# Kernel optimization log

Measured on AMD Instinct MI355X. Metric: run time of the kernel, lower is better.

## Reference

```python
import jax, jax.numpy as jnp
import numpy as np

B, N, E = 4, 1024, 16
S = 4  # num species
AH = PH = 64  # hidden dims


def _mlp(x, W0, b0, W1, b1, W2, b2):
    h = jax.nn.silu(x @ W0 + b0)
    h = jax.nn.silu(h @ W1 + b1)
    return h @ W2 + b2  # [..., 1]


def setup_inputs() -> dict:
    key = jax.random.key(0)
    ks = jax.random.split(key, 20)
    scale = 0.1
    inp = {
        "positions": jax.random.normal(ks[0], (B, N, 2), jnp.float32),
        "species": jax.random.randint(ks[1], (B, N), 0, S, jnp.int32),
        "electric_field": jax.random.normal(ks[2], (B, 2), jnp.float32),
        "embed": jax.random.normal(ks[3], (S, E), jnp.float32) * scale,
        "aW0": jax.random.normal(ks[4], (2 + 2 + 1 + E, AH), jnp.float32) * scale,
        "ab0": jax.random.normal(ks[5], (AH,), jnp.float32) * scale,
        "aW1": jax.random.normal(ks[6], (AH, AH), jnp.float32) * scale,
        "ab1": jax.random.normal(ks[7], (AH,), jnp.float32) * scale,
        "aW2": jax.random.normal(ks[8], (AH, 1), jnp.float32) * scale,
        "ab2": jax.random.normal(ks[9], (1,), jnp.float32) * scale,
        "pW0": jax.random.normal(ks[10], (2 + 1 + 1 + 1 + 2 * E, PH), jnp.float32) * scale,
        "pb0": jax.random.normal(ks[11], (PH,), jnp.float32) * scale,
        "pW1": jax.random.normal(ks[12], (PH, PH), jnp.float32) * scale,
        "pb1": jax.random.normal(ks[13], (PH,), jnp.float32) * scale,
        "pW2": jax.random.normal(ks[14], (PH, 1), jnp.float32) * scale,
        "pb2": jax.random.normal(ks[15], (1,), jnp.float32) * scale,
    }
    return inp


def reference(positions, species, electric_field, embed,
              aW0, ab0, aW1, ab1, aW2, ab2,
              pW0, pb0, pW1, pb1, pW2, pb2):
    num_atoms = positions.shape[1]
    cp = positions - positions.mean(axis=1, keepdims=True)         # [B,N,2]
    semb = embed[species]                                          # [B,N,E]
    e_norm = jnp.linalg.norm(electric_field, axis=-1, keepdims=True)  # [B,1]

    # atom channel
    atom_field = jnp.broadcast_to(electric_field[:, None, :], (cp.shape[0], num_atoms, 2))
    atom_enorm = jnp.broadcast_to(e_norm[:, None, :], (cp.shape[0], num_atoms, 1))
    atom_feat = jnp.concatenate([cp, atom_field, atom_enorm, semb], axis=-1)
    atom_energy = _mlp(atom_feat, aW0, ab0, aW1, ab1, aW2, ab2)[..., 0].sum(axis=1)

    # pair channel: all i<j pairs, fully vectorized
    i_idx, j_idx = jnp.triu_indices(num_atoms, k=1)                # [P]
    rij = cp[:, i_idx, :] - cp[:, j_idx, :]                        # [B,P,2]
    dij = jnp.linalg.norm(rij, axis=-1, keepdims=True)             # [B,P,1]
    uij = rij / jnp.maximum(dij, 1e-12)
    e_dot_u = jnp.sum(electric_field[:, None, :] * uij, axis=-1, keepdims=True)
    pair_enorm = jnp.broadcast_to(e_norm[:, None, :], dij.shape)
    pair_feat = jnp.concatenate(
        [rij, dij, e_dot_u, pair_enorm, semb[:, i_idx, :], semb[:, j_idx, :]], axis=-1)
    pair_energy = _mlp(pair_feat, pW0, pb0, pW1, pb1, pW2, pb2)[..., 0].sum(axis=1)

    return atom_energy + pair_energy
```

## Files before the change

kernel.cpp:

```cpp
#include <hip/hip_runtime.h>

#define NA 1024
#define NBATCH 4
#define NPAIR 523776
#define PAIR_TILES 2046
#define PAIR_BLOCKS 511
#define GRID_X 512

#define LOG2E_F 1.44269504088896f
#define LN2_F   0.69314718055995f

#define WS_MEAN 0
#define WS_W0P  64
#define WS_W0A  2112
#define WS_W1P  4160
#define WS_W1A  12352

typedef _Float16 half4 __attribute__((ext_vector_type(4)));
typedef _Float16 half8 __attribute__((ext_vector_type(8)));
typedef __fp16 fp16x2 __attribute__((ext_vector_type(2)));
typedef float float4v __attribute__((ext_vector_type(4)));

#if defined(__has_builtin)
#  if __has_builtin(__builtin_amdgcn_exp2f)
#    define EXP2F(x) __builtin_amdgcn_exp2f(x)
#  endif
#endif
#ifndef EXP2F
#  define EXP2F(x) exp2f(x)
#endif

__device__ __forceinline__ float4v sig4(float4v y) {
    float4v e;
#pragma unroll
    for (int r = 0; r < 4; r++) e[r] = EXP2F(-y[r]);
    float4v d = e + 1.0f;
    float4v rr;
#pragma unroll
    for (int r = 0; r < 4; r++) rr[r] = __builtin_amdgcn_rcpf(d[r]);
    return rr;
}

__device__ __forceinline__ uint32_t pkf16(float a, float b) {
    union { _Float16 h[2]; uint32_t u; } x;
    x.h[0] = (_Float16)a; x.h[1] = (_Float16)b;
    return x.u;
}

__global__ void prep_kernel(const float* __restrict__ positions,
                            const float* __restrict__ embed,
                            const float* __restrict__ aW0,
                            const float* __restrict__ ab0,
                            const float* __restrict__ aW1,
                            const float* __restrict__ ab2,
                            const float* __restrict__ pW0,
                            const float* __restrict__ pb0,
                            const float* __restrict__ pW1,
                            const float* __restrict__ pb2,
                            char* __restrict__ ws,
                            float* __restrict__ out) {
    const int tid = threadIdx.x;
    if (blockIdx.x < 4) {
        const int b = blockIdx.x;
        const float2* pos = (const float2*)positions + b * NA;
        float sx = 0.f, sy = 0.f;
        for (int t = tid; t < NA; t += 256) {
            float2 p = pos[t];
            sx += p.x; sy += p.y;
        }
#pragma unroll
        for (int off = 32; off > 0; off >>= 1) {
            sx += __shfl_down(sx, off);
            sy += __shfl_down(sy, off);
        }
        __shared__ float rxs[4], rys[4];
        const int w = tid >> 6, lane = tid & 63;
        if (lane == 0) { rxs[w] = sx; rys[w] = sy; }
        __syncthreads();
        if (tid == 0) {
            float* meanws = (float*)(ws + WS_MEAN);
            meanws[b * 2 + 0] = (rxs[0] + rxs[1] + rxs[2] + rxs[3]) * (1.f / NA);
            meanws[b * 2 + 1] = (rys[0] + rys[1] + rys[2] + rys[3]) * (1.f / NA);
            out[b] = (float)NPAIR * pb2[0] + (float)NA * ab2[0];
        }
        return;
    }

    _Float16* w0p = (_Float16*)(ws + WS_W0P);
    _Float16* w0a = (_Float16*)(ws + WS_W0A);
    _Float16* w1p = (_Float16*)(ws + WS_W1P);
    _Float16* w1a = (_Float16*)(ws + WS_W1A);

    for (int idx = tid; idx < 1024; idx += 256) {
        const int j = idx & 3, lane = (idx >> 2) & 63, nt = idx >> 8;
        const int k = ((lane >> 4) << 2) + j;
        const int col = nt * 16 + (lane & 15);
        float vp = 0.f, va = 0.f;
        if (k < 5) {
            vp = pW0[k * 64 + col];
            va = aW0[k * 64 + col];
        } else if (k == 5) {
            vp = pb0[col];
            va = ab0[col];
        } else if (k >= 6 && k <= 9) {
            const int s = k - 6;
            float accp = 0.f, acca = 0.f;
#pragma unroll
            for (int e = 0; e < 16; e++) {
                float em = embed[s * 16 + e];
                accp += em * pW0[(5 + e) * 64 + col];
                acca += em * aW0[(5 + e) * 64 + col];
            }
            vp = accp; va = acca;
        } else if (k >= 10 && k <= 13) {
            const int s = k - 10;
            float accp = 0.f;
#pragma unroll
            for (int e = 0; e < 16; e++)
                accp += embed[s * 16 + e] * pW0[(21 + e) * 64 + col];
            vp = accp; va = 0.f;
        }
        w0p[idx] = (_Float16)(vp * LOG2E_F);
        w0a[idx] = (_Float16)(va * LOG2E_F);
    }
    for (int idx = tid; idx < 4096; idx += 256) {
        const int j = idx & 7, lane = (idx >> 3) & 63;
        const int ks = (idx >> 9) & 1, nt = idx >> 10;
        const int q = lane >> 4;
        const int m = (j < 4) ? (4 * q + j) : (16 + 4 * q + (j - 4));
        const int k = ks * 32 + m;
        const int col = nt * 16 + (lane & 15);
        w1p[idx] = (_Float16)pW1[k * 64 + col];
        w1a[idx] = (_Float16)aW1[k * 64 + col];
    }
}

__global__ __launch_bounds__(256, 4) void mlp_kernel(
    const float* __restrict__ positions,
    const int*   __restrict__ species,
    const float* __restrict__ efield,
    const float* __restrict__ ab1, const float* __restrict__ aW2,
    const float* __restrict__ pb1, const float* __restrict__ pW2,
    const char*  __restrict__ ws,
    float* __restrict__ out)
{
    const int b    = blockIdx.y;
    const int bx   = blockIdx.x;
    const bool is_atom = (bx == PAIR_BLOCKS);
    const int tid  = threadIdx.x;
    const int lane = tid & 63;
    const int wv   = tid >> 6;
    const int n16  = lane & 15;
    const int quad = lane >> 4;

    __shared__ __attribute__((aligned(16))) _Float16 Xbuf[4][64][24];
    _Float16 (*rows)[24] = Xbuf[wv];

    const _Float16* w0w = (const _Float16*)(ws + (is_atom ? WS_W0A : WS_W0P));
    const _Float16* w1w = (const _Float16*)(ws + (is_atom ? WS_W1A : WS_W1P));
    half4 w0f[4];
    half8 w1f[4][2];
#pragma unroll
    for (int nt = 0; nt < 4; nt++)
        w0f[nt] = *(const half4*)(w0w + (nt * 64 + lane) * 4);
#pragma unroll
    for (int nt = 0; nt < 4; nt++)
#pragma unroll
        for (int ks = 0; ks < 2; ks++)
            w1f[nt][ks] = *(const half8*)(w1w + ((nt * 2 + ks) * 64 + lane) * 8);

    const float* B1 = is_atom ? ab1 : pb1;
    float4v b1q[4];
#pragma unroll
    for (int nt = 0; nt < 4; nt++) {
        float4v t4 = *(const float4v*)(B1 + nt * 16 + quad * 4);
        b1q[nt] = t4 * LOG2E_F;
    }

    const float Ex = efield[b * 2 + 0];
    const float Ey = efield[b * 2 + 1];
    const float enorm = sqrtf(Ex * Ex + Ey * Ey);
    const float* meanws = (const float*)(ws + WS_MEAN);
    const float mnx = meanws[b * 2 + 0];
    const float mny = meanws[b * 2 + 1];

    const uint32_t enorm_pack = pkf16(enorm, 1.0f);
    const uint32_t ef_pack    = pkf16(Ex, Ey);

    const int my_tiles = is_atom ? 4 : ((bx < PAIR_TILES - 4 * PAIR_BLOCKS) ? 5 : 4);

    const float4v zero4 = {0.f, 0.f, 0.f, 0.f};
    float4v acce[4];
#pragma unroll
    for (int nt = 0; nt < 4; nt++) acce[nt] = zero4;

    for (int t = 0; t < my_tiles; ++t) {
        uint32_t w01, w23;
        uint64_t ohi, ohj;
        if (!is_atom) {
            const int tile = bx + t * PAIR_BLOCKS;
            const int p = tile * 256 + tid;
            const float s = sqrtf((float)(2047 * 2047 - 8 * p));
            int i = (int)((2047.0f - s) * 0.5f);
            i = i < 0 ? 0 : (i > 1022 ? 1022 : i);
            const int j = p - ((i * (2047 - i)) >> 1) + i + 1;
            const float2* pos = (const float2*)positions + b * NA;
            float2 pi = pos[i], pj = pos[j];
            float f0 = pi.x - pj.x, f1 = pi.y - pj.y;
            float f2 = sqrtf(f0 * f0 + f1 * f1);
            float inv = __builtin_amdgcn_rcpf(fmaxf(f2, 1e-12f));
            float f3 = (Ex * f0 + Ey * f1) * inv;
            w01 = pkf16(f0, f1);
            w23 = pkf16(f2, f3);
            ohi = 0x3C00ull << (species[b * NA + i] * 16);
            ohj = 0x3C00ull << (species[b * NA + j] * 16);
        } else {
            const int n = t * 256 + tid;
            float2 pn = ((const float2*)positions)[b * NA + n];
            w01 = pkf16(pn.x - mnx, pn.y - mny);
            w23 = ef_pack;
            ohi = 0x3C00ull << (species[b * NA + n] * 16);
            ohj = 0;
        }
        int4* dst = (int4*)&rows[lane][0];
        int4 lo, hi;
        lo.x = (int)w01;
        lo.y = (int)w23;
        lo.z = (int)enorm_pack;
        lo.w = (int)(uint32_t)ohi;
        hi.x = (int)(uint32_t)(ohi >> 32);
        hi.y = (int)(uint32_t)ohj;
        hi.z = (int)(uint32_t)(ohj >> 32);
        hi.w = 0;
        dst[0] = lo;
        dst[1] = hi;

        half4 xfr[4];
#pragma unroll
        for (int mt = 0; mt < 4; mt++)
            xfr[mt] = *(const half4*)(&rows[mt * 16 + n16][quad * 4]);

#pragma unroll
        for (int mt = 0; mt < 4; mt++) {
            float4v acc[4];
#pragma unroll
            for (int nt = 0; nt < 4; nt++)
                acc[nt] = __builtin_amdgcn_mfma_f32_16x16x16f16(
                    w0f[nt], xfr[mt], zero4, 0, 0, 0);

            float4v s0 = acc[0] * sig4(acc[0]);
            float4v s1 = acc[1] * sig4(acc[1]);
            float4v s2 = acc[2] * sig4(acc[2]);
            float4v s3 = acc[3] * sig4(acc[3]);
            union { half8 h8; fp16x2 h2[4]; } u0, u1;
            u0.h2[0] = __builtin_amdgcn_cvt_pkrtz(s0[0], s0[1]);
            u0.h2[1] = __builtin_amdgcn_cvt_pkrtz(s0[2], s0[3]);
            u0.h2[2] = __builtin_amdgcn_cvt_pkrtz(s1[0], s1[1]);
            u0.h2[3] = __builtin_amdgcn_cvt_pkrtz(s1[2], s1[3]);
            u1.h2[0] = __builtin_amdgcn_cvt_pkrtz(s2[0], s2[1]);
            u1.h2[1] = __builtin_amdgcn_cvt_pkrtz(s2[2], s2[3]);
            u1.h2[2] = __builtin_amdgcn_cvt_pkrtz(s3[0], s3[1]);
            u1.h2[3] = __builtin_amdgcn_cvt_pkrtz(s3[2], s3[3]);

#pragma unroll
            for (int nt = 0; nt < 4; nt++) {
                float4v c = b1q[nt];
                c = __builtin_amdgcn_mfma_f32_16x16x32_f16(w1f[nt][0], u0.h8, c, 0, 0, 0);
                c = __builtin_amdgcn_mfma_f32_16x16x32_f16(w1f[nt][1], u1.h8, c, 0, 0, 0);
                acce[nt] += c * sig4(c);
            }
        }
    }

    const float* W2 = is_atom ? aW2 : pW2;
    float4v dot4 = {0.f, 0.f, 0.f, 0.f};
#pragma unroll
    for (int nt = 0; nt < 4; nt++) {
        float4v w2v4 = *(const float4v*)(W2 + nt * 16 + quad * 4);
        dot4 += acce[nt] * w2v4;
    }
    float energy = (dot4[0] + dot4[1] + dot4[2] + dot4[3]) * LN2_F;

#pragma unroll
    for (int off = 32; off > 0; off >>= 1)
        energy += __shfl_down(energy, off);
    __shared__ float wsum[4];
    if (lane == 0) wsum[wv] = energy;
    __syncthreads();
    if (tid == 0)
        atomicAdd(&out[b], wsum[0] + wsum[1] + wsum[2] + wsum[3]);
}

extern "C" void kernel_launch(void* const* d_in, const int* in_sizes, int n_in,
                              void* d_out, int out_size, void* d_ws, size_t ws_size,
                              hipStream_t stream) {
    const float* positions = (const float*)d_in[0];
    const int*   species   = (const int*)  d_in[1];
    const float* efield    = (const float*)d_in[2];
    const float* embed     = (const float*)d_in[3];
    const float* aW0 = (const float*)d_in[4];
    const float* ab0 = (const float*)d_in[5];
    const float* aW1 = (const float*)d_in[6];
    const float* ab1 = (const float*)d_in[7];
    const float* aW2 = (const float*)d_in[8];
    const float* ab2 = (const float*)d_in[9];
    const float* pW0 = (const float*)d_in[10];
    const float* pb0 = (const float*)d_in[11];
    const float* pW1 = (const float*)d_in[12];
    const float* pb1 = (const float*)d_in[13];
    const float* pW2 = (const float*)d_in[14];
    const float* pb2 = (const float*)d_in[15];
    float* outp = (float*)d_out;
    char*  ws   = (char*)d_ws;

    prep_kernel<<<dim3(5), dim3(256), 0, stream>>>(
        positions, embed, aW0, ab0, aW1, ab2, pW0, pb0, pW1, pb2, ws, outp);
    mlp_kernel<<<dim3(GRID_X, NBATCH), dim3(256), 0, stream>>>(
        positions, species, efield,
        ab1, aW2, pb1, pW2,
        ws, outp);
}
```

Baseline: 152.7 us.

## Software-pipeline pair tile loads and LDS staging across MLP compute

Restructures the tile loop so the global loads of positions and species for the next tile are issued before the current tile's MFMA work. The LDS row write and fragment reads for that next tile are interleaved between the per-row-block MLP bodies, overlapping memory latency with matrix and sigmoid math. It also replaces the packed round-toward-zero f16 conversions with plain casts. In exchange it keeps more registers live per thread, which could lower occupancy, and the new casts may emit more conversion instructions.

```diff
diff --git a/kernel.cpp b/kernel.cpp
--- a/kernel.cpp
+++ b/kernel.cpp
@@ -18,7 +18,6 @@
 
 typedef _Float16 half4 __attribute__((ext_vector_type(4)));
 typedef _Float16 half8 __attribute__((ext_vector_type(8)));
-typedef __fp16 fp16x2 __attribute__((ext_vector_type(2)));
 typedef float float4v __attribute__((ext_vector_type(4)));
 
 #if defined(__has_builtin)
@@ -184,6 +183,9 @@
     const float mnx = meanws[b * 2 + 0];
     const float mny = meanws[b * 2 + 1];
 
+    const float2* pos = (const float2*)positions + b * NA;
+    const int*    spc = species + b * NA;
+
     const uint32_t enorm_pack = pkf16(enorm, 1.0f);
     const uint32_t ef_pack    = pkf16(Ex, Ey);
 
@@ -194,83 +196,106 @@
 #pragma unroll
     for (int nt = 0; nt < 4; nt++) acce[nt] = zero4;
 
+    half4 xfr[4];
+
+#define LOADRAW(TT, o_pi, o_pj, o_si, o_sj) do {                              \
+        if (!is_atom) {                                                       \
+            const int p_ = (bx + (TT) * PAIR_BLOCKS) * 256 + tid;             \
+            const float sq_ = sqrtf((float)(2047 * 2047 - 8 * p_));           \
+            int i_ = (int)((2047.0f - sq_) * 0.5f);                           \
+            i_ = i_ < 0 ? 0 : (i_ > 1022 ? 1022 : i_);                        \
+            const int j_ = p_ - ((i_ * (2047 - i_)) >> 1) + i_ + 1;           \
+            o_pi = pos[i_]; o_pj = pos[j_];                                   \
+            o_si = spc[i_]; o_sj = spc[j_];                                   \
+        } else {                                                              \
+            const int n_ = (TT) * 256 + tid;                                  \
+            o_pi = pos[n_]; o_si = spc[n_];                                   \
+        }                                                                     \
+    } while (0)
+
+#define PACKWRITE(i_pi, i_pj, i_si, i_sj) do {                                \
+        uint32_t w01_, w23_; uint64_t ohi_, ohj_;                             \
+        if (!is_atom) {                                                       \
+            float f0_ = i_pi.x - i_pj.x, f1_ = i_pi.y - i_pj.y;               \
+            float f2_ = sqrtf(f0_ * f0_ + f1_ * f1_);                         \
+            float inv_ = __builtin_amdgcn_rcpf(fmaxf(f2_, 1e-12f));           \
+            float f3_ = (Ex * f0_ + Ey * f1_) * inv_;                         \
+            w01_ = pkf16(f0_, f1_); w23_ = pkf16(f2_, f3_);                   \
+            ohi_ = 0x3C00ull << (i_si * 16);                                  \
+            ohj_ = 0x3C00ull << (i_sj * 16);                                  \
+        } else {                                                              \
+            w01_ = pkf16(i_pi.x - mnx, i_pi.y - mny);                         \
+            w23_ = ef_pack;                                                   \
+            ohi_ = 0x3C00ull << (i_si * 16);                                  \
+            ohj_ = 0;                                                         \
+        }                                                                     \
+        int4* dst_ = (int4*)&rows[lane][0];                                   \
+        int4 lo_, hi_;                                                        \
+        lo_.x = (int)w01_; lo_.y = (int)w23_;                                 \
+        lo_.z = (int)enorm_pack; lo_.w = (int)(uint32_t)ohi_;                 \
+        hi_.x = (int)(uint32_t)(ohi_ >> 32); hi_.y = (int)(uint32_t)ohj_;     \
+        hi_.z = (int)(uint32_t)(ohj_ >> 32); hi_.w = 0;                       \
+        dst_[0] = lo_; dst_[1] = hi_;                                         \
+    } while (0)
+
+#define READXFR_ONE(MT)                                                       \
+    xfr[MT] = *(const half4*)(&rows[(MT) * 16 + n16][quad * 4])
+
+#define MTBODY(MT) do {                                                       \
+        float4v acc_[4];                                                      \
+        _Pragma("unroll")                                                     \
+        for (int nt = 0; nt < 4; nt++)                                        \
+            acc_[nt] = __builtin_amdgcn_mfma_f32_16x16x16f16(                 \
+                w0f[nt], xfr[MT], zero4, 0, 0, 0);                            \
+        float4v s0_ = acc_[0] * sig4(acc_[0]);                                \
+        float4v s1_ = acc_[1] * sig4(acc_[1]);                                \
+        float4v s2_ = acc_[2] * sig4(acc_[2]);                                \
+        float4v s3_ = acc_[3] * sig4(acc_[3]);                                \
+        half8 h0_, h1_;                                                       \
+        _Pragma("unroll")                                                     \
+        for (int r = 0; r < 4; r++) {                                         \
+            h0_[r]     = (_Float16)s0_[r];                                    \
+            h0_[4 + r] = (_Float16)s1_[r];                                    \
+            h1_[r]     = (_Float16)s2_[r];                                    \
+            h1_[4 + r] = (_Float16)s3_[r];                                    \
+        }                                                                     \
+        _Pragma("unroll")                                                     \
+        for (int nt = 0; nt < 4; nt++) {                                      \
+            float4v c_ = b1q[nt];                                             \
+            c_ = __builtin_amdgcn_mfma_f32_16x16x32_f16(w1f[nt][0], h0_, c_, 0, 0, 0); \
+            c_ = __builtin_amdgcn_mfma_f32_16x16x32_f16(w1f[nt][1], h1_, c_, 0, 0, 0); \
+            acce[nt] += c_ * sig4(c_);                                        \
+        }                                                                     \
+    } while (0)
+
+    {
+        float2 c_pi, c_pj; int c_si = 0, c_sj = 0;
+        LOADRAW(0, c_pi, c_pj, c_si, c_sj);
+        PACKWRITE(c_pi, c_pj, c_si, c_sj);
+        READXFR_ONE(0); READXFR_ONE(1); READXFR_ONE(2); READXFR_ONE(3);
+    }
+
     for (int t = 0; t < my_tiles; ++t) {
-        uint32_t w01, w23;
-        uint64_t ohi, ohj;
-        if (!is_atom) {
-            const int tile = bx + t * PAIR_BLOCKS;
-            const int p = tile * 256 + tid;
-            const float s = sqrtf((float)(2047 * 2047 - 8 * p));
-            int i = (int)((2047.0f - s) * 0.5f);
-            i = i < 0 ? 0 : (i > 1022 ? 1022 : i);
-            const int j = p - ((i * (2047 - i)) >> 1) + i + 1;
-            const float2* pos = (const float2*)positions + b * NA;
-            float2 pi = pos[i], pj = pos[j];
-            float f0 = pi.x - pj.x, f1 = pi.y - pj.y;
-            float f2 = sqrtf(f0 * f0 + f1 * f1);
-            float inv = __builtin_amdgcn_rcpf(fmaxf(f2, 1e-12f));
-            float f3 = (Ex * f0 + Ey * f1) * inv;
-            w01 = pkf16(f0, f1);
-            w23 = pkf16(f2, f3);
-            ohi = 0x3C00ull << (species[b * NA + i] * 16);
-            ohj = 0x3C00ull << (species[b * NA + j] * 16);
-        } else {
-            const int n = t * 256 + tid;
-            float2 pn = ((const float2*)positions)[b * NA + n];
-            w01 = pkf16(pn.x - mnx, pn.y - mny);
-            w23 = ef_pack;
-            ohi = 0x3C00ull << (species[b * NA + n] * 16);
-            ohj = 0;
-        }
-        int4* dst = (int4*)&rows[lane][0];
-        int4 lo, hi;
-        lo.x = (int)w01;
-        lo.y = (int)w23;
-        lo.z = (int)enorm_pack;
-        lo.w = (int)(uint32_t)ohi;
-        hi.x = (int)(uint32_t)(ohi >> 32);
-        hi.y = (int)(uint32_t)ohj;
-        hi.z = (int)(uint32_t)(ohj >> 32);
-        hi.w = 0;
-        dst[0] = lo;
-        dst[1] = hi;
-
-        half4 xfr[4];
-#pragma unroll
-        for (int mt = 0; mt < 4; mt++)
-            xfr[mt] = *(const half4*)(&rows[mt * 16 + n16][quad * 4]);
-
-#pragma unroll
-        for (int mt = 0; mt < 4; mt++) {
-            float4v acc[4];
-#pragma unroll
-            for (int nt = 0; nt < 4; nt++)
-                acc[nt] = __builtin_amdgcn_mfma_f32_16x16x16f16(
-                    w0f[nt], xfr[mt], zero4, 0, 0, 0);
-
-            float4v s0 = acc[0] * sig4(acc[0]);
-            float4v s1 = acc[1] * sig4(acc[1]);
-            float4v s2 = acc[2] * sig4(acc[2]);
-            float4v s3 = acc[3] * sig4(acc[3]);
-            union { half8 h8; fp16x2 h2[4]; } u0, u1;
-            u0.h2[0] = __builtin_amdgcn_cvt_pkrtz(s0[0], s0[1]);
-            u0.h2[1] = __builtin_amdgcn_cvt_pkrtz(s0[2], s0[3]);
-            u0.h2[2] = __builtin_amdgcn_cvt_pkrtz(s1[0], s1[1]);
-            u0.h2[3] = __builtin_amdgcn_cvt_pkrtz(s1[2], s1[3]);
-            u1.h2[0] = __builtin_amdgcn_cvt_pkrtz(s2[0], s2[1]);
-            u1.h2[1] = __builtin_amdgcn_cvt_pkrtz(s2[2], s2[3]);
-            u1.h2[2] = __builtin_amdgcn_cvt_pkrtz(s3[0], s3[1]);
-            u1.h2[3] = __builtin_amdgcn_cvt_pkrtz(s3[2], s3[3]);
-
-#pragma unroll
-            for (int nt = 0; nt < 4; nt++) {
-                float4v c = b1q[nt];
-                c = __builtin_amdgcn_mfma_f32_16x16x32_f16(w1f[nt][0], u0.h8, c, 0, 0, 0);
-                c = __builtin_amdgcn_mfma_f32_16x16x32_f16(w1f[nt][1], u1.h8, c, 0, 0, 0);
-                acce[nt] += c * sig4(c);
-            }
-        }
-    }
+        const bool have_next = (t + 1 < my_tiles);
+        float2 n_pi, n_pj; int n_si = 0, n_sj = 0;
+        if (have_next) LOADRAW(t + 1, n_pi, n_pj, n_si, n_sj);
+
+        MTBODY(0);
+        MTBODY(1);
+        if (have_next) {
+            PACKWRITE(n_pi, n_pj, n_si, n_sj);
+            READXFR_ONE(0); READXFR_ONE(1);
+        }
+        MTBODY(2);
+        if (have_next) READXFR_ONE(2);
+        MTBODY(3);
+        if (have_next) READXFR_ONE(3);
+    }
+
+#undef LOADRAW
+#undef PACKWRITE
+#undef READXFR_ONE
+#undef MTBODY
 
     const float* W2 = is_atom ? aW2 : pW2;
     float4v dot4 = {0.f, 0.f, 0.f, 0.f};
```

New measurement: 172.0 us. 1.13x slower.
